# Performance work log

Measured on AMD Instinct MI355X. Metric: run time of the kernel, lower is better.

Reference implementation:

```python
import jax, jax.numpy as jnp
import numpy as np

EPS = 1e-5


def _conv1x1_3d(x, w, b):
    # x: [B,C,T,H,W], w: [O,C], b: [O]  (Conv3d with kernel 1)
    return jnp.einsum('bcthw,oc->bothw', x, w) + b[None, :, None, None, None]


def _nonlocal_layer(x, Kw, Kb, Qw, Qb, Vw, Vb, Ow, Ob, gamma, beta, in_dim):
    K = _conv1x1_3d(x, Kw, Kb)
    Q = _conv1x1_3d(x, Qw, Qb)
    V = _conv1x1_3d(x, Vw, Vb)
    B, C, T, H, W = K.shape
    S = T * H * W
    Kf = K.reshape(B, C, S)
    Qf = Q.reshape(B, C, S)
    Vf = V.reshape(B, C, S)
    # KQ[b,s,t] = sum_c K[b,c,s] Q[b,c,t];  attn = softmax over t
    attn = jax.nn.softmax(jnp.einsum('bcs,bct->bst', Kf, Qf) / np.sqrt(in_dim).astype(np.float32), axis=2)
    # original broadcast pattern: (V.view(B,C,S,1) * attn[:,None]).sum(3)
    #   == V[b,c,s] * sum_t attn[b,s,t]  (rows of softmax sum to ~1)
    Vn = Vf * attn.sum(axis=2)[:, None, :]
    Vn = jax.nn.relu(Vn).reshape(B, C, T, H, W)
    O = jax.nn.relu(_conv1x1_3d(Vn, Ow, Ob))
    y = x + O
    # BatchNorm3d in training mode: per-channel batch statistics
    mu = y.mean(axis=(0, 2, 3, 4), keepdims=True)
    var = y.var(axis=(0, 2, 3, 4), keepdims=True)
    return gamma[None, :, None, None, None] * (y - mu) / jnp.sqrt(var + EPS) + beta[None, :, None, None, None]


def _conv_transpose_2x2_s2(x, w, b):
    # torch ConvTranspose2d(k=2, stride=2): weight [Cin, Cout, 2, 2]; output pixels don't overlap
    N, C, H, W = x.shape
    O = w.shape[1]
    y = jnp.einsum('nchw,codk->nohdwk', x, w).reshape(N, O, 2 * H, 2 * W)
    return y + b[None, :, None, None]


def _positional_encoding(S, D):
    position = jnp.arange(S, dtype=jnp.float32)[:, None]
    div_term = jnp.exp(jnp.arange(0, D, 2, dtype=jnp.float32) * (-np.log(10000.0) / D))
    pe = jnp.zeros((S, D), dtype=jnp.float32)
    pe = pe.at[:, 0::2].set(jnp.sin(position * div_term))
    pe = pe.at[:, 1::2].set(jnp.cos(position * div_term))
    return pe  # [S, D]


def setup_inputs() -> dict:
    key = jax.random.key(0)
    ks = jax.random.split(key, 24)
    B, Tc, Hc, Wc = 8, 6, 12, 12
    Tf, Hf, Wf = 4, 12, 12
    Din, Dff, Dout, L = 1024, 512, 128, 2
    s = 0.02
    inp = {
        'context': jax.random.normal(ks[0], (B, Tc, Din, Hc, Wc), jnp.float32),
        'frame': jax.random.normal(ks[1], (B, Tf, Din, Hf, Wf), jnp.float32),
        'nl_Kw': jax.random.normal(ks[2], (L, Dff, Din), jnp.float32) * s,
        'nl_Kb': jnp.zeros((L, Dff), jnp.float32),
        'nl_Qw': jax.random.normal(ks[3], (L, Dff, Din), jnp.float32) * s,
        'nl_Qb': jnp.zeros((L, Dff), jnp.float32),
        'nl_Vw': jax.random.normal(ks[4], (L, Dff, Din), jnp.float32) * s,
        'nl_Vb': jnp.zeros((L, Dff), jnp.float32),
        'nl_Ow': jax.random.normal(ks[5], (L, Din, Dff), jnp.float32) * s,
        'nl_Ob': jnp.zeros((L, Din), jnp.float32),
        'nl_gamma': jnp.ones((L, Din), jnp.float32),
        'nl_beta': jnp.zeros((L, Din), jnp.float32),
        'tp_w': jax.random.normal(ks[6], (Dout, Din, 3, 3, 3), jnp.float32) * s,
        'tp_b': jnp.zeros((Dout,), jnp.float32),
        'up1_w': jax.random.normal(ks[7], (Din, Dff, 2, 2), jnp.float32) * s,
        'up1_b': jnp.zeros((Dff,), jnp.float32),
        'up2_w': jax.random.normal(ks[8], (Dff, Dout, 2, 2), jnp.float32) * s,
        'up2_b': jnp.zeros((Dout,), jnp.float32),
    }
    return inp


def reference(context, frame, nl_Kw, nl_Kb, nl_Qw, nl_Qb, nl_Vw, nl_Vb, nl_Ow, nl_Ob,
              nl_gamma, nl_beta, tp_w, tp_b, up1_w, up1_b, up2_w, up2_b):
    in_dim = context.shape[2]
    out_dim = up2_w.shape[1]
    # ---- non-local layers over context ----
    x = jnp.swapaxes(context, 1, 2)  # [B, C, T, H, W]
    n_layers = nl_Kw.shape[0]
    for l in range(n_layers):
        x = _nonlocal_layer(x, nl_Kw[l], nl_Kb[l], nl_Qw[l], nl_Qb[l], nl_Vw[l], nl_Vb[l],
                            nl_Ow[l], nl_Ob[l], nl_gamma[l], nl_beta[l], in_dim)
    # ---- temporal pool (Conv3d k=3, VALID) + ReLU + global avg pool ----
    g = jax.lax.conv_general_dilated(x, tp_w, (1, 1, 1), 'VALID',
                                     dimension_numbers=('NCDHW', 'OIDHW', 'NCDHW'))
    g = jax.nn.relu(g + tp_b[None, :, None, None, None])
    goal_embed = g.mean(axis=(2, 3, 4))  # [B, out_dim]
    # ---- upsample frame ----
    B, Tf, C, H, W = frame.shape
    fr = frame.reshape(B * Tf, C, H, W)
    h = jax.nn.relu(_conv_transpose_2x2_s2(fr, up1_w, up1_b))
    h = _conv_transpose_2x2_s2(h, up2_w, up2_b)  # [B*Tf, out_dim, 4H, 4W]
    N = B * Tf
    S = H * W * 16
    state_embed = h.reshape(N, out_dim, S)
    # ---- positional encoding on V ----
    pe = _positional_encoding(S, out_dim)  # [S, D]
    V = jnp.transpose(state_embed, (0, 2, 1)) + pe[None, :, :]  # [N, S, D]
    # ---- goal/state attention (note: torch .repeat tiles t-major, kept faithful) ----
    goal_rep = jnp.tile(goal_embed, (Tf, 1))  # [Tf*B, D], index t*B+b
    SG = jnp.einsum('nds,nd->ns', state_embed, goal_rep) / np.sqrt(out_dim).astype(np.float32)
    attn = jax.nn.softmax(SG, axis=1)  # [N, S]
    state_goal_attn = jnp.einsum('ns,nsd->nd', attn, V).reshape(B, Tf, out_dim)
    return (goal_embed, state_goal_attn)
```

## Files before the change

### kernel.cpp

```cpp
#include <hip/hip_runtime.h>
#include <cstddef>
#include <cstdint>


static constexpr int B_ = 8, TC = 6, TF = 4, DIN = 1024, DFF = 512, DOUT = 128;
static constexpr int HWP = 144;
static constexpr int P_CTX = B_ * TC * HWP;
static constexpr int NF = B_ * TF;
static constexpr int P_FRM = NF * HWP;
static constexpr int P_H1 = NF * 24 * 24;
static constexpr int P_H2 = NF * 48 * 48;
static constexpr int S2 = 48 * 48;
static constexpr int NPOS = 3200;

static constexpr size_t OFF_XB   = 0;
static constexpr size_t OFF_YB   = 3538944;
static constexpr size_t OFF_VNB  = 7077888;
static constexpr size_t OFF_WB1  = 8847360;
static constexpr size_t OFF_WB2  = 9371648;
static constexpr size_t OFF_TWB  = 9900032;
static constexpr size_t OFF_W1B  = 11669504;
static constexpr size_t OFF_W2B  = 12718080;
static constexpr size_t OFF_ST   = 12849152;
static constexpr size_t OFF_GP   = 12849152;
static constexpr size_t OFF_R    = 18378752;
static constexpr size_t OFF_HP1B = 18788352;
static constexpr size_t OFF_F0B  = 23506944;
static constexpr size_t OFF_HP2B = 0;
static constexpr size_t OFF_SG   = 14692352;
static constexpr size_t OFF_PE   = 7077888;

typedef __attribute__((ext_vector_type(8))) short bf16x8;
typedef __attribute__((ext_vector_type(4))) float f32x4;
typedef __attribute__((ext_vector_type(4))) unsigned short us4;
typedef __attribute__((ext_vector_type(8))) unsigned short us8;

__device__ __forceinline__ unsigned short f2b(float f) {
    union { float f; uint32_t u; } x{f};
    uint32_t r = x.u + 0x7FFFu + ((x.u >> 16) & 1u);
    return (unsigned short)(r >> 16);
}
__device__ __forceinline__ float b2f(unsigned short u) {
    union { uint32_t u; float f; } x;
    x.u = (uint32_t)u << 16;
    return x.f;
}

#define GL16(g, s)                                                        \
    __builtin_amdgcn_global_load_lds(                                     \
        (const __attribute__((address_space(1))) void*)(g),               \
        (__attribute__((address_space(3))) void*)(s), 16, 0, 0)

static constexpr int PW0 = 4 * 524288;
static constexpr int PW1 = PW0 + 27 * 1024 * 128;
static constexpr int PW2 = PW1 + 4 * 512 * 1024;
static constexpr int PW3 = PW2 + 4 * 128 * 512;
static constexpr int NB_PREP = PW3 / 256;
static constexpr int NB_CTXT = 9 * 16 * (B_ * TC);
static constexpr int NB_FRMT = 9 * 16 * NF;
static constexpr int NB_STZ  = 32;

__device__ __forceinline__ void transpose_body(const float* __restrict__ in,
                                               unsigned short* __restrict__ outB,
                                               int C, int HW, int bx, int by, int bz,
                                               float (*T)[17]) {
    int tid = threadIdx.x;
    int tx = tid & 15, ty = tid >> 4;
    int f = bz, hw0 = bx * 16, c0 = by * 64;
#pragma unroll
    for (int i = 0; i < 4; ++i)
        T[ty + 16 * i][tx] = in[((size_t)f * C + c0 + ty + 16 * i) * HW + hw0 + tx];
    __syncthreads();
#pragma unroll
    for (int i = 0; i < 4; ++i)
        outB[((size_t)f * HW + hw0 + ty) * C + c0 + tx + 16 * i] = f2b(T[tx + 16 * i][ty]);
}

__global__ __launch_bounds__(256) void prep_all(
    const float* __restrict__ Vw, const float* __restrict__ Ow,
    const float* __restrict__ tp, const float* __restrict__ u1w,
    const float* __restrict__ u2w,
    const float* __restrict__ context, const float* __restrict__ frame,
    unsigned short* __restrict__ WB1, unsigned short* __restrict__ WB2,
    unsigned short* __restrict__ TWB, unsigned short* __restrict__ W1B,
    unsigned short* __restrict__ W2B,
    unsigned short* __restrict__ XB, unsigned short* __restrict__ F0B,
    float* __restrict__ ST) {
    __shared__ float T[64][17];
    int b = blockIdx.x;
    if (b < NB_PREP) {
        int t = b * 256 + threadIdx.x;
        if (t < PW0) {
            int which = t >> 19;
            int r = t & 524287;
            int kr = r & 7;
            int layer = which >> 1;
            if ((which & 1) == 0) {
                int o = (r >> 3) & 511, kg = (r >> 3) >> 9;
                WB1[(size_t)layer * 524288 + r] =
                    f2b(Vw[(size_t)layer * 524288 + (size_t)o * 1024 + kg * 8 + kr]);
            } else {
                int o = (r >> 3) & 1023, kg = (r >> 3) >> 10;
                WB2[(size_t)layer * 524288 + r] =
                    f2b(Ow[(size_t)layer * 524288 + (size_t)o * 512 + kg * 8 + kr]);
            }
        } else if (t < PW1) {
            int r = t - PW0;
            int kr = r & 7, o = (r >> 3) & 127, kg = (r >> 10) & 127, tap = r >> 17;
            int c = kg * 8 + kr;
            TWB[r] = f2b(tp[((size_t)o * 1024 + c) * 27 + tap]);
        } else if (t < PW2) {
            int r = t - PW1;
            int kr = r & 7, o = (r >> 3) % 512;
            int rest = (r >> 3) / 512;
            int kg = rest & 127, d = rest >> 7;
            W1B[r] = f2b(u1w[((size_t)(kg * 8 + kr) * 512 + o) * 4 + d]);
        } else if (t < PW3) {
            int r = t - PW2;
            int kr = r & 7, o = (r >> 3) & 127;
            int rest = (r >> 3) >> 7;
            int kg = rest & 63, d = rest >> 6;
            W2B[r] = f2b(u2w[((size_t)(kg * 8 + kr) * 128 + o) * 4 + d]);
        }
    } else if (b < NB_PREP + NB_CTXT) {
        int bb = b - NB_PREP;
        transpose_body(context, XB, DIN, HWP, bb % 9, (bb / 9) % 16, bb / 144, T);
    } else if (b < NB_PREP + NB_CTXT + NB_FRMT) {
        int bb = b - NB_PREP - NB_CTXT;
        transpose_body(frame, F0B, DIN, HWP, bb % 9, (bb / 9) % 16, bb / 144, T);
    } else {
        int idx = (b - NB_PREP - NB_CTXT - NB_FRMT) * 256 + threadIdx.x;
        ST[idx] = 0.f;
    }
}

template <int EPI, int REMAP, int GATHER, int MT>
__device__ __forceinline__ void gemm_body(
    const unsigned short* __restrict__ A, const unsigned short* __restrict__ Bp,
    const float* __restrict__ bias, const unsigned short* __restrict__ resid,
    void* __restrict__ Cv, float* __restrict__ stats, int M, int N, int K,
    size_t bStrideZ, size_t cStrideZ,
    int inW, int inHW, int outW, int outSPP,
    int bx, int by, int bz,
    unsigned short* AlP, unsigned short* BlP, int* sPix) {
    constexpr int MI = MT / 32;
    constexpr int AL = MT / 64;
    constexpr int ASZ = MT * 32;
    int tid = threadIdx.x;
    int w = tid >> 6, l = tid & 63;
    int m0 = by * MT, n0 = bx * 128;
    int z = bz;
    const unsigned short* Bpz = Bp + (size_t)z * bStrideZ;

    if (GATHER) {
        if (tid < MT) {
            int pos = m0 + tid;
            int ww = pos % 10;
            int r = pos / 10;
            int h = r % 10;
            r /= 10;
            int t = r & 3, b = r >> 2;
            int dt = z / 9, rr = z - dt * 9;
            int doff = dt * 144 + (rr / 3) * 12 + (rr % 3);
            sPix[tid] = ((b * 6 + t) * 12 + h) * 12 + ww + doff;
        }
        __syncthreads();
    }

    int wr = w >> 1, wc = w & 1;
    int l15 = l & 15, lg = l >> 4;

    float bv[4];
#pragma unroll
    for (int ni = 0; ni < 4; ++ni)
        bv[ni] = (EPI & 1) ? bias[n0 + wc * 64 + ni * 16 + l15] : 0.f;
    asm volatile("s_waitcnt vmcnt(0)" ::: "memory");

    const unsigned short* ag[AL];
    int aoff[AL];
#pragma unroll
    for (int a = 0; a < AL; ++a) {
        int row = l + a * 64;
        int grow = GATHER ? sPix[row] : (m0 + row);
        ag[a] = A + (size_t)grow * K + w * 8;
        aoff[a] = (w * MT + row) * 8;
    }
    int bkg = tid >> 7, bn = tid & 127;
    const unsigned short* bg0 = Bpz + ((size_t)bkg * N + n0 + bn) * 8;
    const unsigned short* bg1 = Bpz + ((size_t)(bkg + 2) * N + n0 + bn) * 8;
    const int boff0 = tid * 8, boff1 = (tid + 256) * 8;
    size_t bstep = (size_t)32 * N;

    f32x4 acc[MI][4];
#pragma unroll
    for (int mi = 0; mi < MI; ++mi)
#pragma unroll
        for (int ni = 0; ni < 4; ++ni) acc[mi][ni] = (f32x4){0.f, 0.f, 0.f, 0.f};

    int nt = K >> 5;
#pragma unroll
    for (int a = 0; a < AL; ++a) { GL16(ag[a], &AlP[aoff[a]]); ag[a] += 32; }
    GL16(bg0, &BlP[boff0]);
    GL16(bg1, &BlP[boff1]);
    bg0 += bstep; bg1 += bstep;
#pragma unroll
    for (int a = 0; a < AL; ++a) { GL16(ag[a], &AlP[ASZ + aoff[a]]); ag[a] += 32; }
    GL16(bg0, &BlP[4096 + boff0]);
    GL16(bg1, &BlP[4096 + boff1]);
    bg0 += bstep; bg1 += bstep;

    int bc = 0, sb = 2;
    for (int t = 0; t < nt; ++t) {
        __builtin_amdgcn_s_barrier();
        if (t + 2 < nt) {
#pragma unroll
            for (int a = 0; a < AL; ++a) { GL16(ag[a], &AlP[sb * ASZ + aoff[a]]); ag[a] += 32; }
            GL16(bg0, &BlP[sb * 4096 + boff0]);
            GL16(bg1, &BlP[sb * 4096 + boff1]);
            bg0 += bstep; bg1 += bstep;
            if (MT == 128)
                asm volatile("s_waitcnt vmcnt(8)" ::: "memory");
            else
                asm volatile("s_waitcnt vmcnt(6)" ::: "memory");
        } else if (t + 2 == nt) {
            if (MT == 128)
                asm volatile("s_waitcnt vmcnt(4)" ::: "memory");
            else
                asm volatile("s_waitcnt vmcnt(3)" ::: "memory");
        } else {
            asm volatile("s_waitcnt vmcnt(0)" ::: "memory");
        }
        __builtin_amdgcn_sched_barrier(0);
        bf16x8 af[MI], bf[4];
#pragma unroll
        for (int mi = 0; mi < MI; ++mi)
            af[mi] = *(const bf16x8*)&AlP[bc * ASZ + (lg * MT + wr * (MT / 2) + mi * 16 + l15) * 8];
#pragma unroll
        for (int ni = 0; ni < 4; ++ni)
            bf[ni] = *(const bf16x8*)&BlP[bc * 4096 + (lg * 128 + wc * 64 + ni * 16 + l15) * 8];
        __builtin_amdgcn_s_setprio(1);
#pragma unroll
        for (int mi = 0; mi < MI; ++mi)
#pragma unroll
            for (int ni = 0; ni < 4; ++ni)
                acc[mi][ni] = __builtin_amdgcn_mfma_f32_16x16x32_bf16(
                    af[mi], bf[ni], acc[mi][ni], 0, 0, 0);
        __builtin_amdgcn_s_setprio(0);
        __builtin_amdgcn_sched_barrier(0);
        bc = (bc == 2) ? 0 : bc + 1;
        sb = (sb == 2) ? 0 : sb + 1;
    }

    float* Cf = (float*)Cv + (size_t)z * cStrideZ;
    unsigned short* Cb = (unsigned short*)Cv + (size_t)z * cStrideZ;
    float sacc[4] = {0, 0, 0, 0}, qacc[4] = {0, 0, 0, 0};
#pragma unroll
    for (int mi = 0; mi < MI; ++mi) {
#pragma unroll
        for (int r = 0; r < 4; ++r) {
            int m = m0 + wr * (MT / 2) + mi * 16 + lg * 4 + r;
            int orow = m;
            if (REMAP) {
                int ni_ = m / inHW;
                int rem = m - ni_ * inHW;
                int h = rem / inW, ww = rem - h * inW;
                orow = ni_ * outSPP + (2 * h + (z >> 1)) * outW + (2 * ww + (z & 1));
            }
#pragma unroll
            for (int ni = 0; ni < 4; ++ni) {
                int n = n0 + wc * 64 + ni * 16 + l15;
                float v = acc[mi][ni][r] + bv[ni];
                if (EPI & 2) v = fmaxf(v, 0.f);
                if (EPI & 4) v += b2f(resid[(size_t)m * N + n]);
                if (EPI & 16) { sacc[ni] += v; qacc[ni] += v * v; }
                if (EPI & 8)
                    Cb[(size_t)orow * N + n] = f2b(v);
                else
                    Cf[(size_t)orow * N + n] = v;
            }
        }
    }
    if (EPI & 16) {
        __syncthreads();
        float* sred = (float*)AlP;
        sred[tid] = 0.f;
        __syncthreads();
#pragma unroll
        for (int ni = 0; ni < 4; ++ni) {
            int c = wc * 64 + ni * 16 + l15;
            atomicAdd(&sred[c], sacc[ni]);
            atomicAdd(&sred[128 + c], qacc[ni]);
        }
        __syncthreads();
        if (tid < 128)
            atomicAdd(&stats[n0 + tid], sred[tid]);
        else
            atomicAdd(&stats[1024 + n0 + (tid & 127)], sred[tid]);
    }
}

template <int EPI, int REMAP, int GATHER, int MT>
__global__ __launch_bounds__(256) void gemm_mfma(
    const unsigned short* __restrict__ A, const unsigned short* __restrict__ Bp,
    const float* __restrict__ bias, const unsigned short* __restrict__ resid,
    void* __restrict__ Cv, float* __restrict__ stats, int M, int N, int K,
    size_t bStrideZ, size_t cStrideZ,
    int inW, int inHW, int outW, int outSPP) {
    __shared__ unsigned short Al[3 * MT * 32];
    __shared__ unsigned short Bl[3 * 128 * 32];
    __shared__ int sPix[MT];
    gemm_body<EPI, REMAP, GATHER, MT>(A, Bp, bias, resid, Cv, stats, M, N, K,
                                      bStrideZ, cStrideZ, inW, inHW, outW, outSPP,
                                      blockIdx.x, blockIdx.y, blockIdx.z,
                                      Al, Bl, sPix);
}

__global__ __launch_bounds__(256) void conv3_up1(
    const unsigned short* __restrict__ XB, const unsigned short* __restrict__ TWB,
    unsigned short* __restrict__ GP,
    const unsigned short* __restrict__ F0B, const unsigned short* __restrict__ W1B,
    const float* __restrict__ u1b, unsigned short* __restrict__ HP1B) {
    __shared__ unsigned short Al[3 * 128 * 32];
    __shared__ unsigned short Bl[3 * 128 * 32];
    __shared__ int sPix[128];
    if (blockIdx.x < 680) {
        int xcd = blockIdx.x & 7, k = blockIdx.x >> 3;
        int wcnt = (xcd < 3) ? 85 : 84;
        if (k >= wcnt) return;
        int wk = (xcd < 3) ? xcd * 85 + k : 255 + (xcd - 3) * 84 + k;
        gemm_body<8, 0, 1, 128>(XB, TWB, nullptr, nullptr, GP, nullptr,
                                NPOS, DOUT, DIN,
                                (size_t)DIN / 8 * DOUT * 8, (size_t)NPOS * DOUT,
                                0, 0, 0, 0, 0, wk / 27, wk % 27, Al, Bl, sPix);
    } else {
        int lb = blockIdx.x - 680;
        int wk = (lb & 7) * 72 + (lb >> 3);
        int mt = wk >> 4, rest = wk & 15;
        gemm_body<11, 1, 0, 128>(F0B, W1B, u1b, nullptr, HP1B, nullptr,
                                 P_FRM, DFF, DIN,
                                 (size_t)DIN / 8 * DFF * 8, 0, 12, 144, 24, 576,
                                 rest & 3, mt, rest >> 2, Al, Bl, sPix);
    }
}

__global__ __launch_bounds__(256) void up2_tail(
    const unsigned short* __restrict__ HP1B, const unsigned short* __restrict__ W2B,
    const float* __restrict__ u2b, unsigned short* __restrict__ HP2B,
    const unsigned short* __restrict__ Gp, const float* __restrict__ tpb,
    float* __restrict__ R, float* __restrict__ PE, float* __restrict__ out) {
    __shared__ unsigned short Al[3 * 128 * 32];
    __shared__ unsigned short Bl[3 * 128 * 32];
    __shared__ int sPix[128];
    int b = blockIdx.x;
    if (b < 576) {
        gemm_body<9, 1, 0, 128>(HP1B, W2B, u2b, nullptr, HP2B, nullptr,
                                P_H1, DOUT, DFF,
                                (size_t)DFF / 8 * DOUT * 8, 0, 24, 576, 48, 2304,
                                0, b % 144, b / 144, Al, Bl, sPix);
    } else if (b < 2176) {
        int idx = (b - 576) * 256 + threadIdx.x;
        float s = 0.f;
        for (int tap = 0; tap < 27; ++tap) s += b2f(Gp[(size_t)tap * (NPOS * 128) + idx]);
        R[idx] = fmaxf(s + tpb[idx & 127], 0.f);
    } else if (b < 3328) {
        int idx = (b - 2176) * 256 + threadIdx.x;
        int s = idx >> 7, d = idx & 127;
        float freq = expf(-(float)(d & ~1) * (9.210340371976184f / 128.f));
        float ang = (float)s * freq;
        PE[idx] = (d & 1) ? cosf(ang) : sinf(ang);
    } else {
        int idx = (b - 3328) * 256 + threadIdx.x;
        out[1024 + idx] = 0.f;
    }
}

__global__ __launch_bounds__(128) void goal_reduce(const float* __restrict__ R,
                                                   float* __restrict__ out) {
    int b = blockIdx.x, o = threadIdx.x;
    float s = 0.f;
    for (int i = 0; i < 400; ++i) s += R[(size_t)(b * 400 + i) * 128 + o];
    out[b * 128 + o] = s * (1.f / 400.f);
}

__global__ __launch_bounds__(256) void bn_apply_b(const unsigned short* __restrict__ YB,
                                                  unsigned short* __restrict__ XB,
                                                  const float* __restrict__ st,
                                                  const float* __restrict__ gamma,
                                                  const float* __restrict__ beta) {
    int idx = blockIdx.x * 256 + threadIdx.x;
    int c0 = (idx & 255) << 2;
    const float invn = 1.f / 6912.f;
    us4 y = ((const us4*)YB)[idx];
    us4 o;
#pragma unroll
    for (int j = 0; j < 4; ++j) {
        int c = c0 + j;
        float mean = st[c] * invn;
        float var = st[1024 + c] * invn - mean * mean;
        float sc = gamma[c] * rsqrtf(var + 1e-5f);
        float sh = beta[c] - mean * sc;
        o[j] = f2b(b2f(y[j]) * sc + sh);
    }
    ((us4*)XB)[idx] = o;
}


__global__ __launch_bounds__(256) void attn_logits(const unsigned short* __restrict__ Hp2,
                                                   const float* __restrict__ out,
                                                   float* __restrict__ SG) {
    int n = blockIdx.y;
    int tid = threadIdx.x;
    int s = blockIdx.x * 16 + (tid >> 4);
    int l16 = tid & 15;
    us8 row = *((const us8*)(Hp2 + ((size_t)n * S2 + s) * 128) + l16);
    const float* g = out + (n & 7) * 128 + l16 * 8;
    float dot = 0.f;
#pragma unroll
    for (int i = 0; i < 8; ++i) dot += b2f(row[i]) * g[i];
    dot += __shfl_xor(dot, 1);
    dot += __shfl_xor(dot, 2);
    dot += __shfl_xor(dot, 4);
    dot += __shfl_xor(dot, 8);
    if (l16 == 0) SG[(size_t)n * S2 + s] = dot * 0.0883883476483184f;
}

__global__ __launch_bounds__(256) void attn_pv(const unsigned short* __restrict__ Hp2,
                                               const float* __restrict__ SG,
                                               const float* __restrict__ PE,
                                               float* __restrict__ out) {
    __shared__ float red[256];
    int n = blockIdx.y;
    int sb = blockIdx.x;
    int tid = threadIdx.x;
    const float* att = SG + (size_t)n * S2;
    float lmax = -3.4e38f;
#pragma unroll
    for (int i = 0; i < 9; ++i) lmax = fmaxf(lmax, att[tid + 256 * i]);
    red[tid] = lmax;
    __syncthreads();
    for (int off = 128; off > 0; off >>= 1) {
        if (tid < off) red[tid] = fmaxf(red[tid], red[tid + off]);
        __syncthreads();
    }
    float m = red[0];
    __syncthreads();
    float ls = 0.f;
#pragma unroll
    for (int i = 0; i < 9; ++i) ls += expf(att[tid + 256 * i] - m);
    red[tid] = ls;
    __syncthreads();
    for (int off = 128; off > 0; off >>= 1) {
        if (tid < off) red[tid] += red[tid + off];
        __syncthreads();
    }
    float inv = 1.f / red[0];
    int d = tid & 127, half = tid >> 7;
    int s0 = sb * 128 + half * 64;
    float acc = 0.f;
    for (int i = 0; i < 64; ++i) {
        int s = s0 + i;
        float p = expf(att[s] - m) * inv;
        acc += p * (b2f(Hp2[((size_t)n * S2 + s) * 128 + d]) + PE[(size_t)s * 128 + d]);
    }
    atomicAdd(&out[1024 + n * 128 + d], acc);
}


extern "C" void kernel_launch(void* const* d_in, const int* in_sizes, int n_in,
                              void* d_out, int out_size, void* d_ws, size_t ws_size,
                              hipStream_t stream) {
    const float* context = (const float*)d_in[0];
    const float* frame = (const float*)d_in[1];
    const float* Vw = (const float*)d_in[6];
    const float* Vb = (const float*)d_in[7];
    const float* Ow = (const float*)d_in[8];
    const float* Ob = (const float*)d_in[9];
    const float* gamma = (const float*)d_in[10];
    const float* beta = (const float*)d_in[11];
    const float* tpw = (const float*)d_in[12];
    const float* tpb = (const float*)d_in[13];
    const float* u1w = (const float*)d_in[14];
    const float* u1b = (const float*)d_in[15];
    const float* u2w = (const float*)d_in[16];
    const float* u2b = (const float*)d_in[17];
    float* ws = (float*)d_ws;
    float* out = (float*)d_out;

    unsigned short* XB = (unsigned short*)(ws + OFF_XB);
    unsigned short* YB = (unsigned short*)(ws + OFF_YB);
    unsigned short* VNB = (unsigned short*)(ws + OFF_VNB);
    unsigned short* WB1 = (unsigned short*)(ws + OFF_WB1);
    unsigned short* WB2 = (unsigned short*)(ws + OFF_WB2);
    float* ST = ws + OFF_ST;
    unsigned short* TWB = (unsigned short*)(ws + OFF_TWB);
    unsigned short* W1B = (unsigned short*)(ws + OFF_W1B);
    unsigned short* W2B = (unsigned short*)(ws + OFF_W2B);
    unsigned short* GP = (unsigned short*)(ws + OFF_GP);
    float* R = ws + OFF_R;
    unsigned short* F0B = (unsigned short*)(ws + OFF_F0B);
    unsigned short* HP1B = (unsigned short*)(ws + OFF_HP1B);
    unsigned short* HP2B = (unsigned short*)(ws + OFF_HP2B);
    float* SG = ws + OFF_SG;
    float* PE = ws + OFF_PE;

    prep_all<<<NB_PREP + NB_CTXT + NB_FRMT + NB_STZ, 256, 0, stream>>>(
        Vw, Ow, tpw, u1w, u2w, context, frame, WB1, WB2, TWB, W1B, W2B,
        XB, F0B, ST);

    for (int l = 0; l < 2; ++l) {
        float* STl = ST + (size_t)l * 4096;
        gemm_mfma<11, 0, 0, 64><<<dim3(DFF / 128, P_CTX / 64, 1), 256, 0, stream>>>(
            XB, WB1 + (size_t)l * 524288, Vb + l * DFF, nullptr, VNB, nullptr,
            P_CTX, DFF, DIN, 0, 0, 0, 0, 0, 0);
        gemm_mfma<31, 0, 0, 128><<<dim3(DIN / 128, P_CTX / 128, 1), 256, 0, stream>>>(
            VNB, WB2 + (size_t)l * 524288, Ob + l * DIN, XB, YB, STl,
            P_CTX, DIN, DFF, 0, 0, 0, 0, 0, 0);
        bn_apply_b<<<(P_CTX * DIN / 4) / 256, 256, 0, stream>>>(
            YB, XB, STl, gamma + l * DIN, beta + l * DIN);
    }

    conv3_up1<<<680 + 576, 256, 0, stream>>>(XB, TWB, GP, F0B, W1B, u1b, HP1B);

    up2_tail<<<576 + 1600 + 1152 + 16, 256, 0, stream>>>(HP1B, W2B, u2b, HP2B,
                                                         GP, tpb, R, PE, out);
    goal_reduce<<<8, 128, 0, stream>>>(R, out);

    attn_logits<<<dim3(S2 / 16, NF), 256, 0, stream>>>(HP2B, out, SG);
    attn_pv<<<dim3(18, NF), 256, 0, stream>>>(HP2B, SG, PE, out);
}
```

Before: 263.1 us.

## Fuse goal reduction into up2_tail and merge attention logits with softmax-PV

```diff
diff --git a/kernel.cpp b/kernel.cpp
--- a/kernel.cpp
+++ b/kernel.cpp
@@ -23,11 +23,9 @@
 static constexpr size_t OFF_W2B  = 12718080;
 static constexpr size_t OFF_ST   = 12849152;
 static constexpr size_t OFF_GP   = 12849152;
-static constexpr size_t OFF_R    = 18378752;
 static constexpr size_t OFF_HP1B = 18788352;
 static constexpr size_t OFF_F0B  = 23506944;
 static constexpr size_t OFF_HP2B = 0;
-static constexpr size_t OFF_SG   = 14692352;
 static constexpr size_t OFF_PE   = 7077888;
 
 typedef __attribute__((ext_vector_type(8))) short bf16x8;
@@ -59,6 +57,7 @@
 static constexpr int NB_CTXT = 9 * 16 * (B_ * TC);
 static constexpr int NB_FRMT = 9 * 16 * NF;
 static constexpr int NB_STZ  = 32;
+static constexpr int NB_OUTZ = 20;
 
 __device__ __forceinline__ void transpose_body(const float* __restrict__ in,
                                                unsigned short* __restrict__ outB,
@@ -85,7 +84,7 @@
     unsigned short* __restrict__ TWB, unsigned short* __restrict__ W1B,
     unsigned short* __restrict__ W2B,
     unsigned short* __restrict__ XB, unsigned short* __restrict__ F0B,
-    float* __restrict__ ST) {
+    float* __restrict__ ST, float* __restrict__ out) {
     __shared__ float T[64][17];
     int b = blockIdx.x;
     if (b < NB_PREP) {
@@ -128,9 +127,12 @@
     } else if (b < NB_PREP + NB_CTXT + NB_FRMT) {
         int bb = b - NB_PREP - NB_CTXT;
         transpose_body(frame, F0B, DIN, HWP, bb % 9, (bb / 9) % 16, bb / 144, T);
-    } else {
+    } else if (b < NB_PREP + NB_CTXT + NB_FRMT + NB_STZ) {
         int idx = (b - NB_PREP - NB_CTXT - NB_FRMT) * 256 + threadIdx.x;
         ST[idx] = 0.f;
+    } else {
+        int idx = (b - NB_PREP - NB_CTXT - NB_FRMT - NB_STZ) * 256 + threadIdx.x;
+        out[idx] = 0.f;
     }
 }
 
@@ -347,7 +349,7 @@
     const unsigned short* __restrict__ HP1B, const unsigned short* __restrict__ W2B,
     const float* __restrict__ u2b, unsigned short* __restrict__ HP2B,
     const unsigned short* __restrict__ Gp, const float* __restrict__ tpb,
-    float* __restrict__ R, float* __restrict__ PE, float* __restrict__ out) {
+    float* __restrict__ PE, float* __restrict__ out) {
     __shared__ unsigned short Al[3 * 128 * 32];
     __shared__ unsigned short Bl[3 * 128 * 32];
     __shared__ int sPix[128];
@@ -358,28 +360,26 @@
                                 (size_t)DFF / 8 * DOUT * 8, 0, 24, 576, 48, 2304,
                                 0, b % 144, b / 144, Al, Bl, sPix);
     } else if (b < 2176) {
-        int idx = (b - 576) * 256 + threadIdx.x;
+        int p2 = b - 576;
+        int idx = p2 * 256 + threadIdx.x;
         float s = 0.f;
         for (int tap = 0; tap < 27; ++tap) s += b2f(Gp[(size_t)tap * (NPOS * 128) + idx]);
-        R[idx] = fmaxf(s + tpb[idx & 127], 0.f);
-    } else if (b < 3328) {
+        float v = fmaxf(s + tpb[idx & 127], 0.f) * (1.f / 400.f);
+        float* rr = (float*)Al;
+        rr[threadIdx.x] = v;
+        __syncthreads();
+        if (threadIdx.x < 128) {
+            int batch = (2 * p2) / 400;
+            atomicAdd(&out[batch * 128 + threadIdx.x],
+                      rr[threadIdx.x] + rr[threadIdx.x + 128]);
+        }
+    } else {
         int idx = (b - 2176) * 256 + threadIdx.x;
         int s = idx >> 7, d = idx & 127;
         float freq = expf(-(float)(d & ~1) * (9.210340371976184f / 128.f));
         float ang = (float)s * freq;
         PE[idx] = (d & 1) ? cosf(ang) : sinf(ang);
-    } else {
-        int idx = (b - 3328) * 256 + threadIdx.x;
-        out[1024 + idx] = 0.f;
-    }
-}
-
-__global__ __launch_bounds__(128) void goal_reduce(const float* __restrict__ R,
-                                                   float* __restrict__ out) {
-    int b = blockIdx.x, o = threadIdx.x;
-    float s = 0.f;
-    for (int i = 0; i < 400; ++i) s += R[(size_t)(b * 400 + i) * 128 + o];
-    out[b * 128 + o] = s * (1.f / 400.f);
+    }
 }
 
 __global__ __launch_bounds__(256) void bn_apply_b(const unsigned short* __restrict__ YB,
@@ -404,38 +404,36 @@
     ((us4*)XB)[idx] = o;
 }
 
-
-__global__ __launch_bounds__(256) void attn_logits(const unsigned short* __restrict__ Hp2,
-                                                   const float* __restrict__ out,
-                                                   float* __restrict__ SG) {
-    int n = blockIdx.y;
+__global__ __launch_bounds__(256) void attn_fused(
+    const unsigned short* __restrict__ Hp2, const float* __restrict__ PE,
+    float* __restrict__ out) {
+    __shared__ float sGoal[128];
+    __shared__ float sAtt[S2];
+    __shared__ float red[256];
+    int lb = blockIdx.x;
+    int wk = (lb & 7) * 72 + (lb >> 3);
+    int n = wk / 18, sb = wk % 18;
     int tid = threadIdx.x;
-    int s = blockIdx.x * 16 + (tid >> 4);
-    int l16 = tid & 15;
-    us8 row = *((const us8*)(Hp2 + ((size_t)n * S2 + s) * 128) + l16);
-    const float* g = out + (n & 7) * 128 + l16 * 8;
-    float dot = 0.f;
-#pragma unroll
-    for (int i = 0; i < 8; ++i) dot += b2f(row[i]) * g[i];
-    dot += __shfl_xor(dot, 1);
-    dot += __shfl_xor(dot, 2);
-    dot += __shfl_xor(dot, 4);
-    dot += __shfl_xor(dot, 8);
-    if (l16 == 0) SG[(size_t)n * S2 + s] = dot * 0.0883883476483184f;
-}
-
-__global__ __launch_bounds__(256) void attn_pv(const unsigned short* __restrict__ Hp2,
-                                               const float* __restrict__ SG,
-                                               const float* __restrict__ PE,
-                                               float* __restrict__ out) {
-    __shared__ float red[256];
-    int n = blockIdx.y;
-    int sb = blockIdx.x;
-    int tid = threadIdx.x;
-    const float* att = SG + (size_t)n * S2;
+    if (tid < 128) sGoal[tid] = out[(n & 7) * 128 + tid];
+    __syncthreads();
+    const float scale = 0.0883883476483184f;
+#pragma unroll
+    for (int i = 0; i < 9; ++i) {
+        int s = tid + 256 * i;
+        const us8* row = (const us8*)(Hp2 + ((size_t)n * S2 + s) * 128);
+        float dot = 0.f;
+#pragma unroll
+        for (int q = 0; q < 16; ++q) {
+            us8 v = row[q];
+#pragma unroll
+            for (int j = 0; j < 8; ++j) dot += b2f(v[j]) * sGoal[q * 8 + j];
+        }
+        sAtt[s] = dot * scale;
+    }
+    __syncthreads();
     float lmax = -3.4e38f;
 #pragma unroll
-    for (int i = 0; i < 9; ++i) lmax = fmaxf(lmax, att[tid + 256 * i]);
+    for (int i = 0; i < 9; ++i) lmax = fmaxf(lmax, sAtt[tid + 256 * i]);
     red[tid] = lmax;
     __syncthreads();
     for (int off = 128; off > 0; off >>= 1) {
@@ -446,7 +444,7 @@
     __syncthreads();
     float ls = 0.f;
 #pragma unroll
-    for (int i = 0; i < 9; ++i) ls += expf(att[tid + 256 * i] - m);
+    for (int i = 0; i < 9; ++i) ls += expf(sAtt[tid + 256 * i] - m);
     red[tid] = ls;
     __syncthreads();
     for (int off = 128; off > 0; off >>= 1) {
@@ -459,7 +457,7 @@
     float acc = 0.f;
     for (int i = 0; i < 64; ++i) {
         int s = s0 + i;
-        float p = expf(att[s] - m) * inv;
+        float p = expf(sAtt[s] - m) * inv;
         acc += p * (b2f(Hp2[((size_t)n * S2 + s) * 128 + d]) + PE[(size_t)s * 128 + d]);
     }
     atomicAdd(&out[1024 + n * 128 + d], acc);
@@ -496,16 +494,14 @@
     unsigned short* W1B = (unsigned short*)(ws + OFF_W1B);
     unsigned short* W2B = (unsigned short*)(ws + OFF_W2B);
     unsigned short* GP = (unsigned short*)(ws + OFF_GP);
-    float* R = ws + OFF_R;
     unsigned short* F0B = (unsigned short*)(ws + OFF_F0B);
     unsigned short* HP1B = (unsigned short*)(ws + OFF_HP1B);
     unsigned short* HP2B = (unsigned short*)(ws + OFF_HP2B);
-    float* SG = ws + OFF_SG;
     float* PE = ws + OFF_PE;
 
-    prep_all<<<NB_PREP + NB_CTXT + NB_FRMT + NB_STZ, 256, 0, stream>>>(
+    prep_all<<<NB_PREP + NB_CTXT + NB_FRMT + NB_STZ + NB_OUTZ, 256, 0, stream>>>(
         Vw, Ow, tpw, u1w, u2w, context, frame, WB1, WB2, TWB, W1B, W2B,
-        XB, F0B, ST);
+        XB, F0B, ST, out);
 
     for (int l = 0; l < 2; ++l) {
         float* STl = ST + (size_t)l * 4096;
@@ -521,10 +517,8 @@
 
     conv3_up1<<<680 + 576, 256, 0, stream>>>(XB, TWB, GP, F0B, W1B, u1b, HP1B);
 
-    up2_tail<<<576 + 1600 + 1152 + 16, 256, 0, stream>>>(HP1B, W2B, u2b, HP2B,
-                                                         GP, tpb, R, PE, out);
-    goal_reduce<<<8, 128, 0, stream>>>(R, out);
-
-    attn_logits<<<dim3(S2 / 16, NF), 256, 0, stream>>>(HP2B, out, SG);
-    attn_pv<<<dim3(18, NF), 256, 0, stream>>>(HP2B, SG, PE, out);
-}
+    up2_tail<<<576 + 1600 + 1152, 256, 0, stream>>>(HP1B, W2B, u2b, HP2B,
+                                                    GP, tpb, PE, out);
+
+    attn_fused<<<576, 256, 0, stream>>>(HP2B, PE, out);
+}
```

Result: slower. 381.2 us (+44.9%).
